# Performance work log

Measured on AMD Instinct MI355X. Metric: run time of the kernel, lower is better.

## Reference

```python
import jax, jax.numpy as jnp
import numpy as np

_J6 = jnp.array([[0, 0, 0, 0, 0, 1], [0, 0, 0, 0, -1, 0], [0, 0, 0, 1, 0, 0],
                 [0, 0, 1, 0, 0, 0], [0, -1, 0, 0, 0, 0], [1, 0, 0, 0, 0, 0]], dtype=jnp.float32)
_PAIRS4 = [(0, 1), (0, 2), (0, 3), (1, 2), (1, 3), (2, 3)]


def exterior(p1, p2):
    # p1, p2: (B,T,H,4) -> (B,T,H,6) normalized Pluecker line coordinates
    parts = [p1[..., i] * p2[..., j] - p1[..., j] * p2[..., i] for i, j in _PAIRS4]
    L = jnp.stack(parts, axis=-1)
    n = jnp.sqrt(jnp.sum(L * L, axis=-1, keepdims=True))
    return L / jnp.maximum(n, 1e-12)


def setup_inputs() -> dict:
    D, H = 1024, 16
    B, T = 2, 2048
    key = jax.random.key(0)
    ks = jax.random.split(key, 16)
    s = 0.02
    return {
        'x': jax.random.normal(ks[0], (B, T, D), dtype=jnp.float32),
        'qkv_w': jax.random.normal(ks[1], (D, 3 * D), dtype=jnp.float32) * s,
        'qkv_b': jnp.zeros((3 * D,), dtype=jnp.float32),
        'w1_write': jax.random.normal(ks[2], (D, 4 * H), dtype=jnp.float32) * s,
        'w2_write': jax.random.normal(ks[3], (D, 4 * H), dtype=jnp.float32) * s,
        'w1_read': jax.random.normal(ks[4], (D, 4 * H), dtype=jnp.float32) * s,
        'w2_read': jax.random.normal(ks[5], (D, 4 * H), dtype=jnp.float32) * s,
        'geo_w': jax.random.normal(ks[6], (D, D), dtype=jnp.float32) * s,
        'geo_b': jnp.zeros((D,), dtype=jnp.float32),
        'gate_w': jax.random.normal(ks[7], (D, H), dtype=jnp.float32) * s,
        'gate_b': jnp.zeros((H,), dtype=jnp.float32),
        'inc_scale': jnp.ones((H,), dtype=jnp.float32),
        'out_w': jax.random.normal(ks[8], (D, D), dtype=jnp.float32) * s,
        'out_b': jnp.zeros((D,), dtype=jnp.float32),
    }


def reference(x, qkv_w, qkv_b, w1_write, w2_write, w1_read, w2_read,
              geo_w, geo_b, gate_w, gate_b, inc_scale, out_w, out_b):
    B, T, D = x.shape
    H = inc_scale.shape[0]
    dh = D // H
    scale = dh ** -0.5

    qkv = (x @ qkv_w + qkv_b).reshape(B, T, 3, H, dh)
    qkv = jnp.transpose(qkv, (2, 0, 3, 1, 4))  # (3,B,H,T,dh)
    q, k, v = qkv[0], qkv[1], qkv[2]

    std_logits = jnp.einsum('bhqd,bhkd->bhqk', q, k) * scale

    x_prev = jnp.concatenate([jnp.zeros((B, 1, D), dtype=x.dtype), x[:, :-1]], axis=1)
    w1 = (x_prev @ w1_write).reshape(B, T, H, 4)
    w2 = (x @ w2_write).reshape(B, T, H, 4)
    write_lines = exterior(w1, w2)  # (B,T,H,6)
    r1 = (x @ w1_read).reshape(B, T, H, 4)
    r2 = (x @ w2_read).reshape(B, T, H, 4)
    read_lines = exterior(r1, r2)  # (B,T,H,6)

    J_write = jnp.einsum('bthi,ij->bthj', write_lines, _J6)  # (B,T,H,6)
    geo_logits = jnp.einsum('bqhi,bkhi->bhqk', read_lines, J_write)
    geo_logits = geo_logits * inc_scale.reshape(1, H, 1, 1)

    mask = jnp.triu(jnp.ones((T, T), dtype=bool), k=1)  # True above diagonal
    neg = jnp.float32(-jnp.inf)

    std_attn = jax.nn.softmax(jnp.where(mask, neg, std_logits), axis=-1)
    std_out = jnp.einsum('bhqk,bhkd->bqhd', std_attn, v).reshape(B, T, D)

    geo_attn = jax.nn.softmax(jnp.where(mask, neg, geo_logits), axis=-1)
    geo_v = (x @ geo_w + geo_b).reshape(B, T, H, dh)
    geo_out = jnp.einsum('bhqk,bkhd->bqhd', geo_attn, geo_v).reshape(B, T, D)

    gate = jax.nn.sigmoid(x @ gate_w + gate_b)  # (B,T,H)
    gate = jnp.mean(gate, axis=-1, keepdims=True)  # (B,T,1)

    combined = (1.0 - gate) * std_out + gate * geo_out
    return combined @ out_w + out_b
```

## Files before the change

### kernel.cpp

```cpp
#include <hip/hip_runtime.h>
#include <hip/hip_bf16.h>

#define Bc 2
#define Tc 2048
#define Dc 1024
#define Hc 16
#define Mc (Bc*Tc)
#define QB 64
#define KB 32
#define NALL 4480

typedef __attribute__((ext_vector_type(8))) short bf16x8;
typedef __attribute__((ext_vector_type(4))) short bf16x4;
typedef __attribute__((ext_vector_type(4))) float fx4;

__device__ __forceinline__ short f2bf(float f) {
  __hip_bfloat16 h = __float2bfloat16(f);
  return *reinterpret_cast<short*>(&h);
}
__device__ __forceinline__ float bf2f(short s) {
  unsigned int u = ((unsigned int)(unsigned short)s) << 16;
  float f;
  __builtin_memcpy(&f, &u, 4);
  return f;
}

#define MFMA(a, b, c) __builtin_amdgcn_mfma_f32_16x16x32_bf16((a), (b), (c), 0, 0, 0)

#define GLD16(G, L) __builtin_amdgcn_global_load_lds( \
    (const __attribute__((address_space(1))) unsigned int*)(G), \
    (__attribute__((address_space(3))) unsigned int*)(L), 16, 0, 0)

__global__ __launch_bounds__(256) void f2b_k(const float* __restrict__ in,
                                             short* __restrict__ out) {
  const int i = blockIdx.x * 256 + threadIdx.x;
  const float4 v = ((const float4*)in)[i];
  bf16x4 o;
  o[0] = f2bf(v.x); o[1] = f2bf(v.y); o[2] = f2bf(v.z); o[3] = f2bf(v.w);
  ((bf16x4*)out)[i] = o;
}

__global__ void biasall_k(const float* __restrict__ qkv_b,
                          const float* __restrict__ geob,
                          const float* __restrict__ gateb,
                          float* __restrict__ ball) {
  const int n = blockIdx.x * 256 + threadIdx.x;
  if (n >= NALL) return;
  float v = 0.f;
  if (n < 1024)      v = qkv_b[n] * 0.125f;
  else if (n < 3072) v = qkv_b[n];
  else if (n < 4096) v = geob[n - 3072];
  else if (n >= 4352 && n < 4368) v = gateb[n - 4352];
  ball[n] = v;
}

__global__ __launch_bounds__(256) void tconv_all_k(
    const float* __restrict__ qkv_w, const float* __restrict__ geow,
    const float* __restrict__ w1w, const float* __restrict__ w2w,
    const float* __restrict__ w1r, const float* __restrict__ w2r,
    const float* __restrict__ gatew, short* __restrict__ wtall)
{
  __shared__ float tile[32][33];
  const int n0 = blockIdx.x * 32, k0 = blockIdx.y * 32;
  const int tx = threadIdx.x & 31, ty = threadIdx.x >> 5;
  const int n = n0 + tx;
  const float* src = nullptr; int ln = 0, sN = 0;
  if (n < 3072)      { src = qkv_w; ln = n;        sN = 3072; }
  else if (n < 4096) { src = geow;  ln = n - 3072; sN = 1024; }
  else if (n < 4160) { src = w1w;   ln = n - 4096; sN = 64; }
  else if (n < 4224) { src = w2w;   ln = n - 4160; sN = 64; }
  else if (n < 4288) { src = w1r;   ln = n - 4224; sN = 64; }
  else if (n < 4352) { src = w2r;   ln = n - 4288; sN = 64; }
  else if (n < 4368) { src = gatew; ln = n - 4352; sN = 16; }
  #pragma unroll
  for (int i = 0; i < 4; i++)
    tile[ty * 4 + i][tx] = src ? src[(size_t)(k0 + ty * 4 + i) * sN + ln] : 0.f;
  __syncthreads();
  #pragma unroll
  for (int i = 0; i < 4; i++) {
    const int nn = n0 + ty * 4 + i;
    const float s = (nn < 1024) ? 0.125f : 1.f;
    wtall[(size_t)nn * 1024 + k0 + tx] = f2bf(tile[tx][ty * 4 + i] * s);
  }
}

__global__ __launch_bounds__(256) void tconv_k(const float* __restrict__ W,
                                               short* __restrict__ Wt,
                                               int K, int N) {
  __shared__ float tile[32][33];
  const int k0 = blockIdx.y * 32, n0 = blockIdx.x * 32;
  const int tx = threadIdx.x & 31, ty = threadIdx.x >> 5;
  #pragma unroll
  for (int i = 0; i < 4; i++)
    tile[ty * 4 + i][tx] = W[(size_t)(k0 + ty * 4 + i) * N + n0 + tx];
  __syncthreads();
  #pragma unroll
  for (int i = 0; i < 4; i++)
    Wt[(size_t)(n0 + ty * 4 + i) * K + k0 + tx] = f2bf(tile[tx][ty * 4 + i]);
}

template<bool BF16_OUT>
__global__ __launch_bounds__(256) void gemm_mfma_k(
    const short* __restrict__ A, const short* __restrict__ Bt,
    const float* __restrict__ bias, void* __restrict__ Cv,
    int M, int N, int K)
{
  __shared__ short As[128][32];
  __shared__ short Bs[128][32];
  const int m0 = blockIdx.y * 128, n0 = blockIdx.x * 128;
  const int tid = threadIdx.x;
  const int wave = tid >> 6, lane = tid & 63;
  const int l15 = lane & 15, lg = lane >> 4;
  const int wm = wave >> 1, wn = wave & 1;
  const int srow = lane >> 2;
  const int schk = (lane & 3) * 8;

  const size_t aBase = (size_t)(m0 + wave * 16 + srow) * K + schk;
  const size_t bBase = (size_t)(n0 + wave * 16 + srow) * K + schk;

  fx4 acc[4][4] = {};

  for (int k0 = 0; k0 < K; k0 += 32) {
    __syncthreads();
    GLD16(&A[aBase + k0],              &As[wave * 16][0]);
    GLD16(&A[aBase + (size_t)64 * K + k0], &As[64 + wave * 16][0]);
    GLD16(&Bt[bBase + k0],             &Bs[wave * 16][0]);
    GLD16(&Bt[bBase + (size_t)64 * K + k0], &Bs[64 + wave * 16][0]);
    __syncthreads();
    bf16x8 af[4], bf[4];
    #pragma unroll
    for (int i = 0; i < 4; i++) {
      af[i] = *(const bf16x8*)&As[wm * 64 + i * 16 + l15][8 * lg];
      bf[i] = *(const bf16x8*)&Bs[wn * 64 + i * 16 + l15][8 * lg];
    }
    #pragma unroll
    for (int i = 0; i < 4; i++)
      #pragma unroll
      for (int j = 0; j < 4; j++)
        acc[i][j] = MFMA(af[i], bf[j], acc[i][j]);
  }

  #pragma unroll
  for (int i = 0; i < 4; i++)
    #pragma unroll
    for (int j = 0; j < 4; j++) {
      const int n = n0 + wn * 64 + j * 16 + l15;
      const float bv = bias ? bias[n] : 0.f;
      #pragma unroll
      for (int rg = 0; rg < 4; rg++) {
        const int m = m0 + wm * 64 + i * 16 + lg * 4 + rg;
        const float v = acc[i][j][rg] + bv;
        if constexpr (BF16_OUT)
          ((short*)Cv)[(size_t)m * N + n] = f2bf(v);
        else
          ((float*)Cv)[(size_t)m * N + n] = v;
      }
    }
}

__device__ __forceinline__ void exterior6(const float a[4], const float c[4], float L[6]) {
  L[0] = a[0]*c[1] - a[1]*c[0];
  L[1] = a[0]*c[2] - a[2]*c[0];
  L[2] = a[0]*c[3] - a[3]*c[0];
  L[3] = a[1]*c[2] - a[2]*c[1];
  L[4] = a[1]*c[3] - a[3]*c[1];
  L[5] = a[2]*c[3] - a[3]*c[2];
}

__device__ __forceinline__ void load4bf(const short* p, float o[4]) {
  const bf16x4 v = *(const bf16x4*)p;
  o[0] = bf2f(v[0]); o[1] = bf2f(v[1]); o[2] = bf2f(v[2]); o[3] = bf2f(v[3]);
}

__global__ void lines_k(const short* __restrict__ allb,
                        const float* __restrict__ incs,
                        short* __restrict__ JWb, short* __restrict__ RLb)
{
  const int idx = blockIdx.x * 256 + threadIdx.x;
  if (idx >= Bc * Tc * Hc) return;
  const int h = idx & 15;
  const int t = (idx >> 4) & (Tc - 1);
  const int b = idx >> 15;
  const size_t row = (size_t)b * Tc + t;
  const size_t lrow = ((size_t)(b * Hc + h) * Tc + t) * 8;

  float a[4] = {0.f, 0.f, 0.f, 0.f};
  float c[4];
  load4bf(&allb[row * NALL + 4160 + h * 4], c);
  if (t > 0) load4bf(&allb[(row - 1) * NALL + 4096 + h * 4], a);

  float L[6];
  exterior6(a, c, L);
  float n = sqrtf(L[0]*L[0] + L[1]*L[1] + L[2]*L[2] + L[3]*L[3] + L[4]*L[4] + L[5]*L[5]);
  float inv = 1.f / fmaxf(n, 1e-12f);
  const float s = incs[h];
  bf16x8 jw;
  jw[0] = f2bf( L[5] * inv * s);
  jw[1] = f2bf(-L[4] * inv * s);
  jw[2] = f2bf( L[3] * inv * s);
  jw[3] = f2bf( L[2] * inv * s);
  jw[4] = f2bf(-L[1] * inv * s);
  jw[5] = f2bf( L[0] * inv * s);
  jw[6] = 0; jw[7] = 0;
  *(bf16x8*)&JWb[lrow] = jw;

  load4bf(&allb[row * NALL + 4224 + h * 4], a);
  load4bf(&allb[row * NALL + 4288 + h * 4], c);
  exterior6(a, c, L);
  n = sqrtf(L[0]*L[0] + L[1]*L[1] + L[2]*L[2] + L[3]*L[3] + L[4]*L[4] + L[5]*L[5]);
  inv = 1.f / fmaxf(n, 1e-12f);
  bf16x8 rl;
  #pragma unroll
  for (int i = 0; i < 6; i++) rl[i] = f2bf(L[i] * inv);
  rl[6] = 0; rl[7] = 0;
  *(bf16x8*)&RLb[lrow] = rl;
}

__global__ void gate_k(const short* __restrict__ allb, float* __restrict__ gate) {
  const int idx = blockIdx.x * 256 + threadIdx.x;
  if (idx >= Mc) return;
  float ssum = 0.f;
  #pragma unroll
  for (int hh = 0; hh < 16; hh++) {
    const float v = bf2f(allb[(size_t)idx * NALL + 4352 + hh]);
    ssum += 1.f / (1.f + __expf(-v));
  }
  gate[idx] = ssum * (1.f / 16.f);
}

#define LOADK(K0, a0, a1, b0, b1) { \
  const size_t rb0 = (size_t)(b * Tc + (K0) + l15) * NALL + 1024 + h * 64; \
  const size_t rb1 = rb0 + (size_t)16 * NALL; \
  a0 = *(const bf16x8*)&allb[rb0 + lg * 8]; \
  a1 = *(const bf16x8*)&allb[rb0 + 32 + lg * 8]; \
  b0 = *(const bf16x8*)&allb[rb1 + lg * 8]; \
  b1 = *(const bf16x8*)&allb[rb1 + 32 + lg * 8]; }

#define LOADJW(K0, j0, j1) { \
  j0 = z8; j1 = z8; \
  if (lg == 0) { \
    j0 = *(const bf16x8*)&JWb[(size_t)(bh * Tc + (K0) + l15) * 8]; \
    j1 = *(const bf16x8*)&JWb[(size_t)(bh * Tc + (K0) + 16 + l15) * 8]; \
  } }

#define LOADVG(K0, vr, gr) { \
  vr = *(const bf16x8*)&allb[(size_t)(b * Tc + (K0) + kk) * NALL + 2048 + h * 64 + dg]; \
  gr = *(const bf16x8*)&allb[(size_t)(b * Tc + (K0) + kk) * NALL + 3072 + h * 64 + dg]; }

#define STAGEVG(CUR, vr, gr) { \
  _Pragma("unroll") for (int j = 0; j < 8; j++) { \
    const int d = dg + j; \
    const int col = ((kc2 ^ ((d >> 3) & 3)) << 3) | kl2; \
    Vt[CUR][d][col] = vr[j]; Gt[CUR][d][col] = gr[j]; \
  } }

#define COMPUTE(K0, CUR, ka0, ka1, kb0, kb1, jw0, jw1) \
  if ((K0) <= qhi) { \
    fx4 z = {0.f, 0.f, 0.f, 0.f}; \
    fx4 sS0, sS1, sG0, sG1; \
    __builtin_amdgcn_s_setprio(1); \
    sS0 = MFMA(qf0, ka0, z); sS0 = MFMA(qf1, ka1, sS0); \
    sS1 = MFMA(qf0, kb0, z); sS1 = MFMA(qf1, kb1, sS1); \
    sG0 = MFMA(rlf, jw0, z); sG1 = MFMA(rlf, jw1, z); \
    __builtin_amdgcn_s_setprio(0); \
    if ((K0) + KB - 1 > q0 + wave * 16) { \
      const int kg0 = (K0) + l15, kg1 = (K0) + 16 + l15; \
      _Pragma("unroll") for (int r = 0; r < 4; r++) { \
        const int qg = q0 + wave * 16 + lg * 4 + r; \
        if (kg0 > qg) { sS0[r] = -1e30f; sG0[r] = -1e30f; } \
        if (kg1 > qg) { sS1[r] = -1e30f; sG1[r] = -1e30f; } \
      } } \
    _Pragma("unroll") for (int r = 0; r < 4; r++) { \
      const int ql = lg * 4 + r; \
      const float p0 = __expf(sS0[r]); const float p1 = __expf(sS1[r]); \
      lpS[r] += p0 + p1; \
      Ps[wave][ql][l15] = f2bf(p0); Ps[wave][ql][16 + l15] = f2bf(p1); \
      const float g0 = __expf(sG0[r]); const float g1 = __expf(sG1[r]); \
      lpG[r] += g0 + g1; \
      Pg[wave][ql][l15] = f2bf(g0); Pg[wave][ql][16 + l15] = f2bf(g1); \
    } \
    const bf16x8 pa  = *(const bf16x8*)&Ps[wave][l15][8 * lg]; \
    const bf16x8 pga = *(const bf16x8*)&Pg[wave][l15][8 * lg]; \
    __builtin_amdgcn_s_setprio(1); \
    _Pragma("unroll") for (int dt = 0; dt < 4; dt++) { \
      const int dV = dt * 16 + l15; \
      const int swz = 8 * (lg ^ ((dV >> 3) & 3)); \
      accS[dt] = MFMA(pa,  *(const bf16x8*)&Vt[CUR][dV][swz], accS[dt]); \
      accG[dt] = MFMA(pga, *(const bf16x8*)&Gt[CUR][dV][swz], accG[dt]); \
    } \
    __builtin_amdgcn_s_setprio(0); \
  }

__global__ __launch_bounds__(256) void attn3_k(
    const short* __restrict__ allb,
    const short* __restrict__ RLb,
    const short* __restrict__ JWb,
    const float* __restrict__ gate,
    short* __restrict__ combb)
{
  const int orig = blockIdx.x;
  const int xcd  = orig & 7;
  const int idx  = orig >> 3;
  const int pairIdx = idx & 15;
  const int bh   = xcd + 8 * (idx >> 4);
  const int b = bh >> 4, h = bh & 15;
  const int tid = threadIdx.x;
  const int wave = tid >> 6;
  const int lane = tid & 63;
  const int l15 = lane & 15;
  const int lg  = lane >> 4;
  const int kk  = tid >> 3;
  const int dg  = (tid & 7) * 8;
  const int kc2 = kk >> 3, kl2 = kk & 7;

  __shared__ short Vt[2][64][40];
  __shared__ short Gt[2][64][40];
  __shared__ short Ps[4][16][40];
  __shared__ short Pg[4][16][40];

  const bf16x8 z8 = {0, 0, 0, 0, 0, 0, 0, 0};

  for (int half = 0; half < 2; half++) {
    const int qt = half ? (31 - pairIdx) : pairIdx;
    const int q0 = qt * QB;
    const int nkt = 2 * qt + 2;
    const int qrow = wave * 16 + l15;
    const int qhi = q0 + wave * 16 + 15;

    const size_t qrb = (size_t)(b * Tc + q0 + qrow) * NALL + h * 64;
    const bf16x8 qf0 = *(const bf16x8*)&allb[qrb + lg * 8];
    const bf16x8 qf1 = *(const bf16x8*)&allb[qrb + 32 + lg * 8];
    bf16x8 rlf = z8;
    if (lg == 0) rlf = *(const bf16x8*)&RLb[(size_t)(bh * Tc + q0 + qrow) * 8];

    fx4 accS[4] = {}, accG[4] = {};
    float lpS[4] = {0.f, 0.f, 0.f, 0.f};
    float lpG[4] = {0.f, 0.f, 0.f, 0.f};

    bf16x8 kA0a, kA1a, kB0a, kB1a, jw0a, jw1a, vrA, grA;
    bf16x8 kA0b, kA1b, kB0b, kB1b, jw0b, jw1b, vrB, grB;
    LOADK(0, kA0a, kA1a, kB0a, kB1a);
    LOADJW(0, jw0a, jw1a);
    LOADVG(0, vrA, grA);

    __syncthreads();

    for (int kt = 0; kt < nkt; kt += 2) {
      const int k0a = kt * KB, k0b = k0a + KB;
      STAGEVG(0, vrA, grA);
      LOADK(k0b, kA0b, kA1b, kB0b, kB1b);
      LOADJW(k0b, jw0b, jw1b);
      LOADVG(k0b, vrB, grB);
      __syncthreads();
      COMPUTE(k0a, 0, kA0a, kA1a, kB0a, kB1a, jw0a, jw1a);
      STAGEVG(1, vrB, grB);
      if (kt + 2 < nkt) {
        LOADK(k0b + KB, kA0a, kA1a, kB0a, kB1a);
        LOADJW(k0b + KB, jw0a, jw1a);
        LOADVG(k0b + KB, vrA, grA);
      }
      __syncthreads();
      COMPUTE(k0b, 1, kA0b, kA1b, kB0b, kB1b, jw0b, jw1b);
    }

    #pragma unroll
    for (int r = 0; r < 4; r++) {
      float ls = lpS[r];
      ls += __shfl_xor(ls, 1); ls += __shfl_xor(ls, 2);
      ls += __shfl_xor(ls, 4); ls += __shfl_xor(ls, 8);
      float lgeo = lpG[r];
      lgeo += __shfl_xor(lgeo, 1); lgeo += __shfl_xor(lgeo, 2);
      lgeo += __shfl_xor(lgeo, 4); lgeo += __shfl_xor(lgeo, 8);
      const int qg = q0 + wave * 16 + lg * 4 + r;
      const float gt = gate[(size_t)b * Tc + qg];
      const float invS = (1.f - gt) / ls;
      const float invG = gt / lgeo;
      #pragma unroll
      for (int dt = 0; dt < 4; dt++) {
        const float o = accS[dt][r] * invS + accG[dt][r] * invG;
        combb[(size_t)(b * Tc + qg) * 1024 + h * 64 + dt * 16 + l15] = f2bf(o);
      }
    }
  }
}

extern "C" void kernel_launch(void* const* d_in, const int* in_sizes, int n_in,
                              void* d_out, int out_size, void* d_ws, size_t ws_size,
                              hipStream_t stream) {
  (void)in_sizes; (void)n_in; (void)out_size; (void)ws_size;
  const float* x     = (const float*)d_in[0];
  const float* qkv_w = (const float*)d_in[1];
  const float* qkv_b = (const float*)d_in[2];
  const float* w1w   = (const float*)d_in[3];
  const float* w2w   = (const float*)d_in[4];
  const float* w1r   = (const float*)d_in[5];
  const float* w2r   = (const float*)d_in[6];
  const float* geow  = (const float*)d_in[7];
  const float* geob  = (const float*)d_in[8];
  const float* gatew = (const float*)d_in[9];
  const float* gateb = (const float*)d_in[10];
  const float* incs  = (const float*)d_in[11];
  const float* outw  = (const float*)d_in[12];
  const float* outb  = (const float*)d_in[13];
  float* out = (float*)d_out;

  char* p = (char*)d_ws;
  short* xb    = (short*)p;  p += (size_t)4096 * 1024 * 2;
  short* wtall = (short*)p;  p += (size_t)NALL * 1024 * 2;
  short* allb  = (short*)p;  p += (size_t)4096 * NALL * 2;
  short* combb = (short*)p;  p += (size_t)4096 * 1024 * 2;
  short* wtout = (short*)p;  p += (size_t)1024 * 1024 * 2;
  short* JWb   = (short*)p;  p += (size_t)32 * 2048 * 8 * 2;
  short* RLb   = (short*)p;  p += (size_t)32 * 2048 * 8 * 2;
  float* ball  = (float*)p;  p += (size_t)NALL * 4;
  float* gatev = (float*)p;  p += (size_t)4096 * 4;

  const dim3 blk(256);

  f2b_k<<<dim3(4096), blk, 0, stream>>>(x, xb);
  biasall_k<<<dim3((NALL + 255) / 256), blk, 0, stream>>>(qkv_b, geob, gateb, ball);
  tconv_all_k<<<dim3(NALL / 32, 32), blk, 0, stream>>>(qkv_w, geow, w1w, w2w, w1r, w2r, gatew, wtall);
  tconv_k<<<dim3(32, 32), blk, 0, stream>>>(outw, wtout, 1024, 1024);

  gemm_mfma_k<true><<<dim3(NALL / 128, 32), blk, 0, stream>>>(xb, wtall, ball, allb, 4096, NALL, 1024);

  lines_k<<<dim3((Bc * Tc * Hc + 255) / 256), blk, 0, stream>>>(allb, incs, JWb, RLb);
  gate_k<<<dim3((Mc + 255) / 256), blk, 0, stream>>>(allb, gatev);

  attn3_k<<<dim3(512), blk, 0, stream>>>(allb, RLb, JWb, gatev, combb);

  gemm_mfma_k<false><<<dim3(8, 32), blk, 0, stream>>>(combb, wtout, outb, (void*)out, 4096, 1024, 1024);
}
```

Baseline: 210.7 us.

## Use 64-row tile GEMM for output projection, fold gate into lines, cheaper bf16 rounding

Adds a GEMM kernel with 64x128 tiles for the final output projection, doubling the grid to 512 blocks so more CUs are busy on the small 4096x1024 problem. The gate computation moves into lines_k, removing one kernel launch. The softmax probability bf16 conversion is replaced with a simple add-and-shift rounding that skips NaN and tie handling. The smaller tiles lower per-block data reuse, and the new GEMM has no double buffering.

New measurement: 203.9 us. 3.2% less time.

```diff
diff --git a/kernel.cpp b/kernel.cpp
--- a/kernel.cpp
+++ b/kernel.cpp
@@ -23,6 +23,11 @@
   float f;
   __builtin_memcpy(&f, &u, 4);
   return f;
+}
+__device__ __forceinline__ short p2bf(float f) {
+  unsigned int u;
+  __builtin_memcpy(&u, &f, 4);
+  return (short)((u + 0x8000u) >> 16);
 }
 
 #define MFMA(a, b, c) __builtin_amdgcn_mfma_f32_16x16x32_bf16((a), (b), (c), 0, 0, 0)
@@ -158,6 +163,64 @@
     }
 }
 
+template<bool BF16_OUT>
+__global__ __launch_bounds__(256) void gemm_mfma64_k(
+    const short* __restrict__ A, const short* __restrict__ Bt,
+    const float* __restrict__ bias, void* __restrict__ Cv,
+    int M, int N, int K)
+{
+  __shared__ short As[64][32];
+  __shared__ short Bs[128][32];
+  const int m0 = blockIdx.y * 64, n0 = blockIdx.x * 128;
+  const int tid = threadIdx.x;
+  const int wave = tid >> 6, lane = tid & 63;
+  const int l15 = lane & 15, lg = lane >> 4;
+  const int srow = lane >> 2;
+  const int schk = (lane & 3) * 8;
+
+  const size_t aBase = (size_t)(m0 + wave * 16 + srow) * K + schk;
+  const size_t bBase = (size_t)(n0 + wave * 16 + srow) * K + schk;
+
+  fx4 acc[4][2] = {};
+
+  for (int k0 = 0; k0 < K; k0 += 32) {
+    __syncthreads();
+    GLD16(&A[aBase + k0],                   &As[wave * 16][0]);
+    GLD16(&Bt[bBase + k0],                  &Bs[wave * 16][0]);
+    GLD16(&Bt[bBase + (size_t)64 * K + k0], &Bs[64 + wave * 16][0]);
+    __syncthreads();
+    bf16x8 af[4], bf[2];
+    #pragma unroll
+    for (int i = 0; i < 4; i++)
+      af[i] = *(const bf16x8*)&As[i * 16 + l15][8 * lg];
+    #pragma unroll
+    for (int j = 0; j < 2; j++)
+      bf[j] = *(const bf16x8*)&Bs[wave * 32 + j * 16 + l15][8 * lg];
+    #pragma unroll
+    for (int i = 0; i < 4; i++)
+      #pragma unroll
+      for (int j = 0; j < 2; j++)
+        acc[i][j] = MFMA(af[i], bf[j], acc[i][j]);
+  }
+
+  #pragma unroll
+  for (int i = 0; i < 4; i++)
+    #pragma unroll
+    for (int j = 0; j < 2; j++) {
+      const int n = n0 + wave * 32 + j * 16 + l15;
+      const float bv = bias ? bias[n] : 0.f;
+      #pragma unroll
+      for (int rg = 0; rg < 4; rg++) {
+        const int m = m0 + i * 16 + lg * 4 + rg;
+        const float v = acc[i][j][rg] + bv;
+        if constexpr (BF16_OUT)
+          ((short*)Cv)[(size_t)m * N + n] = f2bf(v);
+        else
+          ((float*)Cv)[(size_t)m * N + n] = v;
+      }
+    }
+}
+
 __device__ __forceinline__ void exterior6(const float a[4], const float c[4], float L[6]) {
   L[0] = a[0]*c[1] - a[1]*c[0];
   L[1] = a[0]*c[2] - a[2]*c[0];
@@ -174,7 +237,8 @@
 
 __global__ void lines_k(const short* __restrict__ allb,
                         const float* __restrict__ incs,
-                        short* __restrict__ JWb, short* __restrict__ RLb)
+                        short* __restrict__ JWb, short* __restrict__ RLb,
+                        float* __restrict__ gatev)
 {
   const int idx = blockIdx.x * 256 + threadIdx.x;
   if (idx >= Bc * Tc * Hc) return;
@@ -214,18 +278,16 @@
   for (int i = 0; i < 6; i++) rl[i] = f2bf(L[i] * inv);
   rl[6] = 0; rl[7] = 0;
   *(bf16x8*)&RLb[lrow] = rl;
-}
-
-__global__ void gate_k(const short* __restrict__ allb, float* __restrict__ gate) {
-  const int idx = blockIdx.x * 256 + threadIdx.x;
-  if (idx >= Mc) return;
-  float ssum = 0.f;
-  #pragma unroll
-  for (int hh = 0; hh < 16; hh++) {
-    const float v = bf2f(allb[(size_t)idx * NALL + 4352 + hh]);
-    ssum += 1.f / (1.f + __expf(-v));
-  }
-  gate[idx] = ssum * (1.f / 16.f);
+
+  if (h == 0) {
+    float ssum = 0.f;
+    #pragma unroll
+    for (int hh = 0; hh < 16; hh++) {
+      const float v = bf2f(allb[row * NALL + 4352 + hh]);
+      ssum += 1.f / (1.f + __expf(-v));
+    }
+    gatev[row] = ssum * (1.f / 16.f);
+  }
 }
 
 #define LOADK(K0, a0, a1, b0, b1) { \
@@ -274,10 +336,10 @@
       const int ql = lg * 4 + r; \
       const float p0 = __expf(sS0[r]); const float p1 = __expf(sS1[r]); \
       lpS[r] += p0 + p1; \
-      Ps[wave][ql][l15] = f2bf(p0); Ps[wave][ql][16 + l15] = f2bf(p1); \
+      Ps[wave][ql][l15] = p2bf(p0); Ps[wave][ql][16 + l15] = p2bf(p1); \
       const float g0 = __expf(sG0[r]); const float g1 = __expf(sG1[r]); \
       lpG[r] += g0 + g1; \
-      Pg[wave][ql][l15] = f2bf(g0); Pg[wave][ql][16 + l15] = f2bf(g1); \
+      Pg[wave][ql][l15] = p2bf(g0); Pg[wave][ql][16 + l15] = p2bf(g1); \
     } \
     const bf16x8 pa  = *(const bf16x8*)&Ps[wave][l15][8 * lg]; \
     const bf16x8 pga = *(const bf16x8*)&Pg[wave][l15][8 * lg]; \
@@ -424,10 +486,9 @@
 
   gemm_mfma_k<true><<<dim3(NALL / 128, 32), blk, 0, stream>>>(xb, wtall, ball, allb, 4096, NALL, 1024);
 
-  lines_k<<<dim3((Bc * Tc * Hc + 255) / 256), blk, 0, stream>>>(allb, incs, JWb, RLb);
-  gate_k<<<dim3((Mc + 255) / 256), blk, 0, stream>>>(allb, gatev);
+  lines_k<<<dim3((Bc * Tc * Hc + 255) / 256), blk, 0, stream>>>(allb, incs, JWb, RLb, gatev);
 
   attn3_k<<<dim3(512), blk, 0, stream>>>(allb, RLb, JWb, gatev, combb);
 
-  gemm_mfma_k<false><<<dim3(8, 32), blk, 0, stream>>>(combb, wtout, outb, (void*)out, 4096, 1024, 1024);
-}
+  gemm_mfma64_k<false><<<dim3(8, 64), blk, 0, stream>>>(combb, wtout, outb, (void*)out, 4096, 1024, 1024);
+}
```
